# Kernel optimization log

Measured on AMD Instinct MI355X. Metric: run time of the kernel, lower is better.

The kernel has to match this reference:

```python
import jax, jax.numpy as jnp
import numpy as np

B, C_IN, H, W = 16, 16, 64, 64
C_OUT, KH, KW, DH, DW = 16, 3, 3, 1, 1
OH = (H - KH) // DH + 1  # 62
OW = (W - KW) // DW + 1  # 62


def setup_inputs() -> dict:
    key = jax.random.key(0)
    k1, k2 = jax.random.split(key)
    x = jax.random.normal(k1, (B, C_IN, H, W), dtype=jnp.float32)
    weight = jax.random.normal(k2, (1, C_OUT, C_IN, OH, OW, KH * KW), dtype=jnp.float32)
    return {"x": x, "weight": weight}


def _extract_patches(x):
    # Equivalent to torch unfold(2,kh,dh).unfold(3,kw,dw).view(..., kh*kw):
    # patches[b,c,y,x,k] with k = i*KW + j (row-major over kernel window).
    slabs = [x[:, :, i:i + OH * DH:DH, j:j + OW * DW:DW]
             for i in range(KH) for j in range(KW)]
    return jnp.stack(slabs, axis=-1)  # [B, C_IN, OH, OW, KH*KW]


def reference(x, weight):
    patches = _extract_patches(x)
    # out[b,o,y,x] = sum_{c,k} patches[b,c,y,x,k] * weight[0,o,c,y,x,k]
    out = jnp.einsum('bcyxk,ocyxk->boyx', patches, weight[0])
    return out
```

## Files before the change

kernel.cpp:

```cpp
#include <hip/hip_runtime.h>


#define CIN   16
#define COUT  16
#define HH    64
#define WW    64
#define OHH   62
#define OWW   62

#define WOSTR (CIN * OHH * OWW * 9)
#define WCSTR (OHH * OWW * 9)
#define OROW  388

__device__ __forceinline__ int ldsIdx(int o, int xi, int k) {
    int j = k >> 2;
    int p = (j + xi) % 3;
    return o * OROW + xi * 12 + p * 4 + (k & 3);
}

__global__ __launch_bounds__(512, 1)
void lc2d(const float* __restrict__ xg,
          const float* __restrict__ wg,
          float* __restrict__ outg)
{
    __shared__ float Wl[2][8 * OROW];

    const int tid = threadIdx.x;
    const int y   = blockIdx.x;
    const int xh  = blockIdx.y;
    const int oh  = blockIdx.z;
    const int x0  = xh * 32;
    const int nx  = xh ? (OWW - 32) : 32;
    const int M   = nx * 9 / 2;
    const int tot = 8 * M;

    const int xl  = tid & 31;
    const int og  = (tid >> 5) & 1;
    const int bg  = tid >> 6;
    const int pos = x0 + xl;
    const bool valid = pos < OWW;
    const int xp  = valid ? pos : (OWW - 1);

    int st_o[3], st_fo[3];
    bool st_en[3];
    #pragma unroll
    for (int r = 0; r < 3; ++r) {
        int id = tid + 512 * r;
        st_en[r] = id < tot;
        int idc = st_en[r] ? id : 0;
        int o = idc / M;
        st_o[r]  = o;
        st_fo[r] = 2 * (idc - o * M);
    }
    int wr0[3], wr1[3];
    #pragma unroll
    for (int r = 0; r < 3; ++r) {
        int fo = st_fo[r];
        int xi = fo / 9;
        int k  = fo - xi * 9;
        wr0[r] = ldsIdx(st_o[r], xi, k);
        int xi2 = (k == 8) ? xi + 1 : xi;
        int k2  = (k == 8) ? 0 : k + 1;
        wr1[r] = ldsIdx(st_o[r], xi2, k2);
    }

    const float* wbase = wg + (size_t)oh * 8 * WOSTR + (size_t)(y * OWW + x0) * 9;

    {
        float2 pf[3];
        #pragma unroll
        for (int r = 0; r < 3; ++r)
            if (st_en[r])
                pf[r] = *(const float2*)(wbase + (size_t)st_o[r] * WOSTR + st_fo[r]);
        #pragma unroll
        for (int r = 0; r < 3; ++r) {
            if (st_en[r]) {
                Wl[0][wr0[r]] = pf[r].x;
                Wl[0][wr1[r]] = pf[r].y;
            }
        }
    }
    __syncthreads();

    float acc[4][2];
    #pragma unroll
    for (int t = 0; t < 4; ++t) {
        acc[t][0] = 0.f; acc[t][1] = 0.f;
    }

    const float* xb0 = xg + ((size_t)(bg * 2 + 0) * CIN) * (HH * WW) + (size_t)y * WW + xp;
    const float* xb1 = xg + ((size_t)(bg * 2 + 1) * CIN) * (HH * WW) + (size_t)y * WW + xp;

    const int p0 = (xl % 3) * 4;
    const int p1 = ((xl + 1) % 3) * 4;
    const int p2 = ((xl + 2) % 3) * 4;

    for (int c = 0; c < CIN; ++c) {
        const float* cur = Wl[c & 1];
        float*       nxt = Wl[(c + 1) & 1];

        float2 npf[3];
        if (c + 1 < CIN) {
            #pragma unroll
            for (int r = 0; r < 3; ++r)
                if (st_en[r])
                    npf[r] = *(const float2*)(wbase + (size_t)st_o[r] * WOSTR
                                              + (size_t)(c + 1) * WCSTR + st_fo[r]);
        }

        float xv[2][9];
        {
            const float* xr0 = xb0 + (size_t)c * (HH * WW);
            const float* xr1 = xb1 + (size_t)c * (HH * WW);
            #pragma unroll
            for (int i = 0; i < 3; ++i)
                #pragma unroll
                for (int j = 0; j < 3; ++j) {
                    xv[0][i * 3 + j] = xr0[i * WW + j];
                    xv[1][i * 3 + j] = xr1[i * WW + j];
                }
        }

        #pragma unroll
        for (int t = 0; t < 4; ++t) {
            const int base = (og * 4 + t) * OROW + xl * 12;
            const float4 w0 = *(const float4*)&cur[base + p0];
            const float4 w1 = *(const float4*)&cur[base + p1];
            const float  w8 = cur[base + p2];
            #pragma unroll
            for (int b = 0; b < 2; ++b) {
                float s = acc[t][b];
                s = fmaf(w0.x, xv[b][0], s);
                s = fmaf(w0.y, xv[b][1], s);
                s = fmaf(w0.z, xv[b][2], s);
                s = fmaf(w0.w, xv[b][3], s);
                s = fmaf(w1.x, xv[b][4], s);
                s = fmaf(w1.y, xv[b][5], s);
                s = fmaf(w1.z, xv[b][6], s);
                s = fmaf(w1.w, xv[b][7], s);
                s = fmaf(w8,   xv[b][8], s);
                acc[t][b] = s;
            }
        }

        if (c + 1 < CIN) {
            #pragma unroll
            for (int r = 0; r < 3; ++r) {
                if (st_en[r]) {
                    nxt[wr0[r]] = npf[r].x;
                    nxt[wr1[r]] = npf[r].y;
                }
            }
            __syncthreads();
        }
    }

    if (valid) {
        #pragma unroll
        for (int t = 0; t < 4; ++t) {
            const int o = oh * 8 + og * 4 + t;
            #pragma unroll
            for (int b = 0; b < 2; ++b) {
                const int bb = bg * 2 + b;
                outg[((size_t)(bb * COUT + o) * OHH + y) * OWW + pos] = acc[t][b];
            }
        }
    }
}

extern "C" void kernel_launch(void* const* d_in, const int* in_sizes, int n_in,
                              void* d_out, int out_size, void* d_ws, size_t ws_size,
                              hipStream_t stream) {
    const float* x = (const float*)d_in[0];
    const float* w = (const float*)d_in[1];
    float* out = (float*)d_out;

    dim3 grid(OHH, 2, 2);
    dim3 block(512);
    lc2d<<<grid, block, 0, stream>>>(x, w, out);
}
```

Before: 89.12 us.

## Split batch and input channels across more blocks with atomic accumulation

The grid grows from 248 to 992 blocks by splitting the batch into halves and the input channels into two chunks of 8. Each block is cut to 256 threads, and launch bounds allow several blocks per CU. Partial sums go to the output with atomicAdd, so a separate kernel now zeroes the output first. The input patch loads are also double-buffered in registers. This is meant to raise occupancy and fill the GPU, but each weight tile is now fetched twice (once per batch half), and it adds an extra launch plus atomic traffic.

Measured after the change: 255.8 us. 2.87x slower.

```diff
diff --git a/kernel.cpp b/kernel.cpp
--- a/kernel.cpp
+++ b/kernel.cpp
@@ -7,10 +7,12 @@
 #define WW    64
 #define OHH   62
 #define OWW   62
+#define HW    (HH * WW)
 
 #define WOSTR (CIN * OHH * OWW * 9)
 #define WCSTR (OHH * OWW * 9)
 #define OROW  388
+#define NC    8
 
 __device__ __forceinline__ int ldsIdx(int o, int xi, int k) {
     int j = k >> 2;
@@ -18,7 +20,12 @@
     return o * OROW + xi * 12 + p * 4 + (k & 3);
 }
 
-__global__ __launch_bounds__(512, 1)
+__global__ __launch_bounds__(256, 1)
+void zero_out(float* __restrict__ outg) {
+    ((float4*)outg)[blockIdx.x * 256 + threadIdx.x] = make_float4(0.f, 0.f, 0.f, 0.f);
+}
+
+__global__ __launch_bounds__(256, 4)
 void lc2d(const float* __restrict__ xg,
           const float* __restrict__ wg,
           float* __restrict__ outg)
@@ -27,12 +34,15 @@
 
     const int tid = threadIdx.x;
     const int y   = blockIdx.x;
-    const int xh  = blockIdx.y;
-    const int oh  = blockIdx.z;
+    const int xh  = blockIdx.y & 1;
+    const int bh  = blockIdx.y >> 1;
+    const int oh  = blockIdx.z & 1;
+    const int ch  = blockIdx.z >> 1;
     const int x0  = xh * 32;
     const int nx  = xh ? (OWW - 32) : 32;
     const int M   = nx * 9 / 2;
     const int tot = 8 * M;
+    const int cstart = ch * NC;
 
     const int xl  = tid & 31;
     const int og  = (tid >> 5) & 1;
@@ -41,20 +51,20 @@
     const bool valid = pos < OWW;
     const int xp  = valid ? pos : (OWW - 1);
 
-    int st_o[3], st_fo[3];
-    bool st_en[3];
+    int st_o[5], st_fo[5];
+    bool st_en[5];
     #pragma unroll
-    for (int r = 0; r < 3; ++r) {
-        int id = tid + 512 * r;
+    for (int r = 0; r < 5; ++r) {
+        int id = tid + 256 * r;
         st_en[r] = id < tot;
         int idc = st_en[r] ? id : 0;
         int o = idc / M;
         st_o[r]  = o;
         st_fo[r] = 2 * (idc - o * M);
     }
-    int wr0[3], wr1[3];
+    int wr0[5], wr1[5];
     #pragma unroll
-    for (int r = 0; r < 3; ++r) {
+    for (int r = 0; r < 5; ++r) {
         int fo = st_fo[r];
         int xi = fo / 9;
         int k  = fo - xi * 9;
@@ -64,16 +74,30 @@
         wr1[r] = ldsIdx(st_o[r], xi2, k2);
     }
 
-    const float* wbase = wg + (size_t)oh * 8 * WOSTR + (size_t)(y * OWW + x0) * 9;
+    const float* wbase = wg + (size_t)oh * 8 * WOSTR + (size_t)cstart * WCSTR
+                            + (size_t)(y * OWW + x0) * 9;
 
+    const float* xb0 = xg + ((size_t)(bh * 8 + bg * 2 + 0) * CIN + cstart) * HW
+                          + (size_t)y * WW + xp;
+    const float* xb1 = xg + ((size_t)(bh * 8 + bg * 2 + 1) * CIN + cstart) * HW
+                          + (size_t)y * WW + xp;
+
+    float xva[2][2][9];
     {
-        float2 pf[3];
+        float2 pf[5];
         #pragma unroll
-        for (int r = 0; r < 3; ++r)
+        for (int r = 0; r < 5; ++r)
             if (st_en[r])
                 pf[r] = *(const float2*)(wbase + (size_t)st_o[r] * WOSTR + st_fo[r]);
         #pragma unroll
-        for (int r = 0; r < 3; ++r) {
+        for (int i = 0; i < 3; ++i)
+            #pragma unroll
+            for (int j = 0; j < 3; ++j) {
+                xva[0][0][i * 3 + j] = xb0[i * WW + j];
+                xva[0][1][i * 3 + j] = xb1[i * WW + j];
+            }
+        #pragma unroll
+        for (int r = 0; r < 5; ++r) {
             if (st_en[r]) {
                 Wl[0][wr0[r]] = pf[r].x;
                 Wl[0][wr1[r]] = pf[r].y;
@@ -84,43 +108,36 @@
 
     float acc[4][2];
     #pragma unroll
-    for (int t = 0; t < 4; ++t) {
-        acc[t][0] = 0.f; acc[t][1] = 0.f;
-    }
-
-    const float* xb0 = xg + ((size_t)(bg * 2 + 0) * CIN) * (HH * WW) + (size_t)y * WW + xp;
-    const float* xb1 = xg + ((size_t)(bg * 2 + 1) * CIN) * (HH * WW) + (size_t)y * WW + xp;
+    for (int t = 0; t < 4; ++t) { acc[t][0] = 0.f; acc[t][1] = 0.f; }
 
     const int p0 = (xl % 3) * 4;
     const int p1 = ((xl + 1) % 3) * 4;
     const int p2 = ((xl + 2) % 3) * 4;
 
-    for (int c = 0; c < CIN; ++c) {
-        const float* cur = Wl[c & 1];
-        float*       nxt = Wl[(c + 1) & 1];
+    #pragma unroll
+    for (int cc = 0; cc < NC; ++cc) {
+        const int cu = cc & 1;
+        const int nu = cu ^ 1;
 
-        float2 npf[3];
-        if (c + 1 < CIN) {
-            #pragma unroll
-            for (int r = 0; r < 3; ++r)
-                if (st_en[r])
-                    npf[r] = *(const float2*)(wbase + (size_t)st_o[r] * WOSTR
-                                              + (size_t)(c + 1) * WCSTR + st_fo[r]);
-        }
-
-        float xv[2][9];
-        {
-            const float* xr0 = xb0 + (size_t)c * (HH * WW);
-            const float* xr1 = xb1 + (size_t)c * (HH * WW);
+        float2 npf[5];
+        if (cc + 1 < NC) {
+            const float* xr0 = xb0 + (size_t)(cc + 1) * HW;
+            const float* xr1 = xb1 + (size_t)(cc + 1) * HW;
             #pragma unroll
             for (int i = 0; i < 3; ++i)
                 #pragma unroll
                 for (int j = 0; j < 3; ++j) {
-                    xv[0][i * 3 + j] = xr0[i * WW + j];
-                    xv[1][i * 3 + j] = xr1[i * WW + j];
+                    xva[nu][0][i * 3 + j] = xr0[i * WW + j];
+                    xva[nu][1][i * 3 + j] = xr1[i * WW + j];
                 }
+            #pragma unroll
+            for (int r = 0; r < 5; ++r)
+                if (st_en[r])
+                    npf[r] = *(const float2*)(wbase + (size_t)st_o[r] * WOSTR
+                                              + (size_t)(cc + 1) * WCSTR + st_fo[r]);
         }
 
+        const float* cur = Wl[cu];
         #pragma unroll
         for (int t = 0; t < 4; ++t) {
             const int base = (og * 4 + t) * OROW + xl * 12;
@@ -130,25 +147,25 @@
             #pragma unroll
             for (int b = 0; b < 2; ++b) {
                 float s = acc[t][b];
-                s = fmaf(w0.x, xv[b][0], s);
-                s = fmaf(w0.y, xv[b][1], s);
-                s = fmaf(w0.z, xv[b][2], s);
-                s = fmaf(w0.w, xv[b][3], s);
-                s = fmaf(w1.x, xv[b][4], s);
-                s = fmaf(w1.y, xv[b][5], s);
-                s = fmaf(w1.z, xv[b][6], s);
-                s = fmaf(w1.w, xv[b][7], s);
-                s = fmaf(w8,   xv[b][8], s);
+                s = fmaf(w0.x, xva[cu][b][0], s);
+                s = fmaf(w0.y, xva[cu][b][1], s);
+                s = fmaf(w0.z, xva[cu][b][2], s);
+                s = fmaf(w0.w, xva[cu][b][3], s);
+                s = fmaf(w1.x, xva[cu][b][4], s);
+                s = fmaf(w1.y, xva[cu][b][5], s);
+                s = fmaf(w1.z, xva[cu][b][6], s);
+                s = fmaf(w1.w, xva[cu][b][7], s);
+                s = fmaf(w8,   xva[cu][b][8], s);
                 acc[t][b] = s;
             }
         }
 
-        if (c + 1 < CIN) {
+        if (cc + 1 < NC) {
             #pragma unroll
-            for (int r = 0; r < 3; ++r) {
+            for (int r = 0; r < 5; ++r) {
                 if (st_en[r]) {
-                    nxt[wr0[r]] = npf[r].x;
-                    nxt[wr1[r]] = npf[r].y;
+                    Wl[nu][wr0[r]] = npf[r].x;
+                    Wl[nu][wr1[r]] = npf[r].y;
                 }
             }
             __syncthreads();
@@ -161,8 +178,9 @@
             const int o = oh * 8 + og * 4 + t;
             #pragma unroll
             for (int b = 0; b < 2; ++b) {
-                const int bb = bg * 2 + b;
-                outg[((size_t)(bb * COUT + o) * OHH + y) * OWW + pos] = acc[t][b];
+                const int bb = bh * 8 + bg * 2 + b;
+                atomicAdd(&outg[((size_t)(bb * COUT + o) * OHH + y) * OWW + pos],
+                          acc[t][b]);
             }
         }
     }
@@ -175,7 +193,7 @@
     const float* w = (const float*)d_in[1];
     float* out = (float*)d_out;
 
-    dim3 grid(OHH, 2, 2);
-    dim3 block(512);
-    lc2d<<<grid, block, 0, stream>>>(x, w, out);
+    zero_out<<<dim3(961), dim3(256), 0, stream>>>(out);
+    dim3 grid(OHH, 4, 4);
+    lc2d<<<grid, dim3(256), 0, stream>>>(x, w, out);
 }
```

## Split input channels across blocks and reduce with atomic adds

Applied to the files above, without the earlier changes.

Splits the 16 input channels into two halves handled by separate blocks, doubling the grid to 496 blocks so more CUs are busy. Partial sums are combined with float atomicAdd into an output buffer that a new kernel zeroes first. Launch bounds now allow up to four 512-thread blocks per CU. The cost is an extra kernel launch, atomic traffic, and a non-deterministic summation order.

Result: slower. 227.9 us (+155.7%).

```diff
diff --git a/kernel.cpp b/kernel.cpp
--- a/kernel.cpp
+++ b/kernel.cpp
@@ -7,10 +7,12 @@
 #define WW    64
 #define OHH   62
 #define OWW   62
+#define HW    (HH * WW)
 
 #define WOSTR (CIN * OHH * OWW * 9)
 #define WCSTR (OHH * OWW * 9)
 #define OROW  388
+#define NC    8
 
 __device__ __forceinline__ int ldsIdx(int o, int xi, int k) {
     int j = k >> 2;
@@ -18,7 +20,12 @@
     return o * OROW + xi * 12 + p * 4 + (k & 3);
 }
 
-__global__ __launch_bounds__(512, 1)
+__global__ __launch_bounds__(256)
+void zero_out(float* __restrict__ outg) {
+    ((float4*)outg)[blockIdx.x * 256 + threadIdx.x] = make_float4(0.f, 0.f, 0.f, 0.f);
+}
+
+__global__ __launch_bounds__(512, 4)
 void lc2d(const float* __restrict__ xg,
           const float* __restrict__ wg,
           float* __restrict__ outg)
@@ -28,11 +35,13 @@
     const int tid = threadIdx.x;
     const int y   = blockIdx.x;
     const int xh  = blockIdx.y;
-    const int oh  = blockIdx.z;
+    const int oh  = blockIdx.z & 1;
+    const int ch  = blockIdx.z >> 1;
     const int x0  = xh * 32;
     const int nx  = xh ? (OWW - 32) : 32;
     const int M   = nx * 9 / 2;
     const int tot = 8 * M;
+    const int cstart = ch * NC;
 
     const int xl  = tid & 31;
     const int og  = (tid >> 5) & 1;
@@ -64,7 +73,8 @@
         wr1[r] = ldsIdx(st_o[r], xi2, k2);
     }
 
-    const float* wbase = wg + (size_t)oh * 8 * WOSTR + (size_t)(y * OWW + x0) * 9;
+    const float* wbase = wg + (size_t)oh * 8 * WOSTR + (size_t)cstart * WCSTR
+                            + (size_t)(y * OWW + x0) * 9;
 
     {
         float2 pf[3];
@@ -84,34 +94,34 @@
 
     float acc[4][2];
     #pragma unroll
-    for (int t = 0; t < 4; ++t) {
-        acc[t][0] = 0.f; acc[t][1] = 0.f;
-    }
+    for (int t = 0; t < 4; ++t) { acc[t][0] = 0.f; acc[t][1] = 0.f; }
 
-    const float* xb0 = xg + ((size_t)(bg * 2 + 0) * CIN) * (HH * WW) + (size_t)y * WW + xp;
-    const float* xb1 = xg + ((size_t)(bg * 2 + 1) * CIN) * (HH * WW) + (size_t)y * WW + xp;
+    const float* xb0 = xg + ((size_t)(bg * 2 + 0) * CIN + cstart) * HW
+                          + (size_t)y * WW + xp;
+    const float* xb1 = xg + ((size_t)(bg * 2 + 1) * CIN + cstart) * HW
+                          + (size_t)y * WW + xp;
 
     const int p0 = (xl % 3) * 4;
     const int p1 = ((xl + 1) % 3) * 4;
     const int p2 = ((xl + 2) % 3) * 4;
 
-    for (int c = 0; c < CIN; ++c) {
-        const float* cur = Wl[c & 1];
-        float*       nxt = Wl[(c + 1) & 1];
+    for (int cc = 0; cc < NC; ++cc) {
+        const float* cur = Wl[cc & 1];
+        float*       nxt = Wl[(cc + 1) & 1];
 
         float2 npf[3];
-        if (c + 1 < CIN) {
+        if (cc + 1 < NC) {
             #pragma unroll
             for (int r = 0; r < 3; ++r)
                 if (st_en[r])
                     npf[r] = *(const float2*)(wbase + (size_t)st_o[r] * WOSTR
-                                              + (size_t)(c + 1) * WCSTR + st_fo[r]);
+                                              + (size_t)(cc + 1) * WCSTR + st_fo[r]);
         }
 
         float xv[2][9];
         {
-            const float* xr0 = xb0 + (size_t)c * (HH * WW);
-            const float* xr1 = xb1 + (size_t)c * (HH * WW);
+            const float* xr0 = xb0 + (size_t)cc * HW;
+            const float* xr1 = xb1 + (size_t)cc * HW;
             #pragma unroll
             for (int i = 0; i < 3; ++i)
                 #pragma unroll
@@ -143,7 +153,7 @@
             }
         }
 
-        if (c + 1 < CIN) {
+        if (cc + 1 < NC) {
             #pragma unroll
             for (int r = 0; r < 3; ++r) {
                 if (st_en[r]) {
@@ -162,7 +172,8 @@
             #pragma unroll
             for (int b = 0; b < 2; ++b) {
                 const int bb = bg * 2 + b;
-                outg[((size_t)(bb * COUT + o) * OHH + y) * OWW + pos] = acc[t][b];
+                atomicAdd(&outg[((size_t)(bb * COUT + o) * OHH + y) * OWW + pos],
+                          acc[t][b]);
             }
         }
     }
@@ -175,7 +186,7 @@
     const float* w = (const float*)d_in[1];
     float* out = (float*)d_out;
 
-    dim3 grid(OHH, 2, 2);
-    dim3 block(512);
-    lc2d<<<grid, block, 0, stream>>>(x, w, out);
+    zero_out<<<dim3(961), dim3(256), 0, stream>>>(out);
+    dim3 grid(OHH, 2, 4);
+    lc2d<<<grid, dim3(512), 0, stream>>>(x, w, out);
 }
```
